# Kernel optimization log

Measured on AMD Instinct MI355X. Metric: run time of the kernel, lower is better.

Reference implementation:

```python
import jax, jax.numpy as jnp
import numpy as np

DIM = 1024
N_STATE = 64
T, B = 512, 32


def _xavier(key, shape):
    fan_out, fan_in = shape
    limit = np.sqrt(6.0 / (fan_in + fan_out)).astype(np.float32)
    return jax.random.uniform(key, shape, jnp.float32, -limit, limit)


def setup_inputs() -> dict:
    key = jax.random.key(0)
    ks = jax.random.split(key, 5)
    return {
        "x": jax.random.normal(ks[0], (T, B, DIM), jnp.float32),
        "S": jnp.zeros((B, N_STATE, N_STATE), jnp.float32),
        "W_k": _xavier(ks[1], (N_STATE, DIM)),
        "W_v": _xavier(ks[2], (N_STATE, DIM)),
        "W_q": _xavier(ks[3], (N_STATE, DIM)),
        "W_alpha": _xavier(ks[4], (N_STATE, DIM)),
        "d_alpha": jnp.full((N_STATE,), 0.1, jnp.float32),
        "b_alpha": jnp.full((N_STATE,), 2.0, jnp.float32),
    }


def reference(x, S, W_k, W_v, W_q, W_alpha, d_alpha, b_alpha):
    # Precompute all projections as batched GEMMs: [T,B,n_state]
    k = jnp.einsum("tbd,nd->tbn", x, W_k)
    v = jnp.einsum("tbd,nd->tbn", x, W_v)
    q = jnp.einsum("tbd,nd->tbn", x, W_q)
    ax = jnp.einsum("tbd,nd->tbn", x, W_alpha)

    def step(S, inp):
        k_t, v_t, q_t, ax_t = inp  # each [B, n_state]
        retrieved = jnp.einsum("bij,bj->bi", S, k_t)          # S @ k
        alpha = jax.nn.sigmoid(ax_t + d_alpha * retrieved + b_alpha)
        # S = alpha * S + (1 - alpha) * outer(v, k); alpha gates rows
        S_new = alpha[:, :, None] * S + (1.0 - alpha)[:, :, None] * (
            v_t[:, :, None] * k_t[:, None, :]
        )
        h = jnp.einsum("bij,bj->bi", S_new, q_t)              # S @ q
        out_t = h * jax.nn.silu(h)                             # self-gated output
        return S_new, out_t

    S_final, output = jax.lax.scan(step, S, (k, v, q, ax))
    return output, S_final
```

## Files before the change

kernel.cpp:

```cpp
#include <hip/hip_runtime.h>
#include <hip/hip_bf16.h>

#define T_STEPS 512
#define BATCH 32
#define NST 64
#define DIM 1024

typedef _Float16 f16x8 __attribute__((ext_vector_type(8)));
typedef _Float16 f16x4 __attribute__((ext_vector_type(4)));
typedef _Float16 f16x2 __attribute__((ext_vector_type(2)));
typedef float f32x4 __attribute__((ext_vector_type(4)));

__device__ __forceinline__ void gl_lds16(const void* g, void* l) {
  __builtin_amdgcn_global_load_lds(
      (const __attribute__((address_space(1))) void*)g,
      (__attribute__((address_space(3))) void*)l, 16, 0, 0);
}

__global__ __launch_bounds__(256) void wconv(
    const float* __restrict__ Wk, const float* __restrict__ Wv,
    const float* __restrict__ Wq, const float* __restrict__ Wa,
    _Float16* __restrict__ Wc) {
  const int n = blockIdx.x;
  const int g = n >> 6, r = n & 63;
  const float* W = (g == 0) ? Wk : (g == 1) ? Wq : (g == 2) ? Wv : Wa;
  float4 v = *(const float4*)(W + (size_t)r * DIM + threadIdx.x * 4);
  f16x4 h = {(_Float16)v.x, (_Float16)v.y, (_Float16)v.z, (_Float16)v.w};
  *(f16x4*)(Wc + (size_t)n * DIM + threadIdx.x * 4) = h;
}

__global__ __launch_bounds__(512) void proj_gemm(
    const float* __restrict__ x, const _Float16* __restrict__ Wc,
    _Float16* __restrict__ projh) {
  const int m0 = blockIdx.x * 64;
  const int tid = threadIdx.x;
  const int lane = tid & 63, wv = tid >> 6;
  const int wm = wv >> 2, wn = wv & 3;
  const int fm = lane & 15, fq = lane >> 4;

  __shared__ __align__(16) _Float16 Bl[2][256 * 32];
  __shared__ __align__(16) _Float16 Al[2][64 * 32];

  const int brow = tid >> 2;
  const int bcg = (tid & 3) ^ ((tid >> 3) & 3);
  const _Float16* gB = Wc + (size_t)brow * DIM + bcg * 8;
  const int bdst = tid * 8;

#define STAGE_B(buf, k0)                                          \
  {                                                               \
    _Pragma("unroll") for (int i = 0; i < 2; ++i)                 \
        gl_lds16(gB + (size_t)i * 128 * DIM + (k0),               \
                 &Bl[buf][i * 4096 + bdst]);                      \
  }

  const int arow = tid >> 3;
  const int afc = (tid & 7) * 4;
  const float* gA = x + (size_t)(m0 + arow) * DIM + afc;
  const int awp = arow * 32 + ((((tid >> 1) & 3) ^ ((arow >> 1) & 3)) * 8) +
                  (tid & 1) * 4;

#define LOADX(rr, k0)                          \
  {                                            \
    rr = *(const float4*)(gA + (k0));          \
  }
#define CVT_WRITE_A(buf, rr)                                        \
  {                                                                 \
    f16x4 h = {(_Float16)rr.x, (_Float16)rr.y, (_Float16)rr.z,      \
               (_Float16)rr.w};                                     \
    *(f16x4*)&Al[buf][awp] = h;                                     \
  }

  f32x4 acc[2][4];
#pragma unroll
  for (int mi = 0; mi < 2; ++mi)
#pragma unroll
    for (int ni = 0; ni < 4; ++ni) acc[mi][ni] = (f32x4){0.f, 0.f, 0.f, 0.f};

  const int aswz = (fq ^ ((fm >> 1) & 3)) * 8;
  const int abase = (wm * 32 + fm) * 32 + aswz;
  const int bbase = (wn * 64 + fm) * 32 + aswz;

#define COMPUTE(cb)                                                     \
  {                                                                     \
    f16x8 afr[2], bfr[4];                                               \
    _Pragma("unroll") for (int mi = 0; mi < 2; ++mi)                    \
        afr[mi] = *(const f16x8*)&Al[cb][abase + mi * 16 * 32];         \
    _Pragma("unroll") for (int ni = 0; ni < 4; ++ni)                    \
        bfr[ni] = *(const f16x8*)&Bl[cb][bbase + ni * 16 * 32];         \
    _Pragma("unroll") for (int mi = 0; mi < 2; ++mi)                    \
        _Pragma("unroll") for (int ni = 0; ni < 4; ++ni)                \
            acc[mi][ni] = __builtin_amdgcn_mfma_f32_16x16x32_f16(       \
                afr[mi], bfr[ni], acc[mi][ni], 0, 0, 0);                \
  }

  float4 rE, rO;
  LOADX(rE, 0);
  STAGE_B(0, 0);
  LOADX(rO, 32);
  CVT_WRITE_A(0, rE);
  __syncthreads();

  for (int k2 = 0; k2 < 16; ++k2) {
    STAGE_B(1, (2 * k2 + 1) * 32);
    if (k2 < 15) LOADX(rE, (2 * k2 + 2) * 32);
    CVT_WRITE_A(1, rO);
    COMPUTE(0);
    __syncthreads();
    if (k2 < 15) {
      STAGE_B(0, (2 * k2 + 2) * 32);
      LOADX(rO, (2 * k2 + 3) * 32);
      CVT_WRITE_A(0, rE);
    }
    COMPUTE(1);
    __syncthreads();
  }
#undef STAGE_B
#undef LOADX
#undef CVT_WRITE_A
#undef COMPUTE

#pragma unroll
  for (int mi = 0; mi < 2; ++mi)
#pragma unroll
    for (int ni = 0; ni < 4; ++ni) {
      const int gcol = wn * 64 + ni * 16 + fm;
      const int pcol = gcol < 128 ? gcol
                     : (gcol < 192 ? 128 + 2 * (gcol - 128) : 129 + 2 * (gcol - 192));
#pragma unroll
      for (int r = 0; r < 4; ++r) {
        const int grow = m0 + wm * 32 + mi * 16 + fq * 4 + r;
        projh[(size_t)grow * 256 + pcol] = (_Float16)acc[mi][ni][r];
      }
    }
}

__device__ __forceinline__ float red16(float x) {
  int v = __builtin_amdgcn_update_dpp(0, __float_as_int(x), 0xB1, 0xF, 0xF, true);
  x += __int_as_float(v);
  v = __builtin_amdgcn_update_dpp(0, __float_as_int(x), 0x4E, 0xF, 0xF, true);
  x += __int_as_float(v);
  v = __builtin_amdgcn_update_dpp(0, __float_as_int(x), 0x124, 0xF, 0xF, true);
  x += __int_as_float(v);
  v = __builtin_amdgcn_update_dpp(0, __float_as_int(x), 0x128, 0xF, 0xF, true);
  x += __int_as_float(v);
  return x;
}

__global__ __launch_bounds__(256) void scan_kernel(
    const _Float16* __restrict__ projh, const float* __restrict__ S0,
    const float* __restrict__ d_alpha, const float* __restrict__ b_alpha,
    float* __restrict__ out, float* __restrict__ Sout) {
  const int b = blockIdx.x >> 2;
  const int rg = blockIdx.x & 3;
  const int tid = threadIdx.x;
  const int c = tid & 15;
  const int r = rg * 16 + (tid >> 4);
  const int j0 = c * 4;

  __shared__ __align__(16) _Float16 lbuf[2 * 2048];

  float s[4];
  {
    float4 v = *(const float4*)(S0 + ((size_t)b * NST + r) * NST + j0);
    s[0] = v.x; s[1] = v.y; s[2] = v.z; s[3] = v.w;
  }
  const float da = d_alpha[r];
  const float ba = b_alpha[r];

  const _Float16* gp = projh + (size_t)b * 256;
  const int lidx = (tid >> 5) * 256 + (tid & 31) * 8;
#define GADDR(ch) (gp + (size_t)((ch) * 8 + (tid >> 5)) * (BATCH * 256) + (tid & 31) * 8)

  float4 rA;
  rA = *(const float4*)GADDR(0); *(float4*)(lbuf + lidx) = rA;
  rA = *(const float4*)GADDR(1); *(float4*)(lbuf + 2048 + lidx) = rA;
  rA = *(const float4*)GADDR(2);
  __syncthreads();

  f16x4 kf[2], qf[2];
  f16x2 vaf[2];
#define PREF(tn)                                                           \
  {                                                                        \
    const int pp = (tn)&1;                                                 \
    const _Float16* Pn = lbuf + (((tn) >> 3) & 1) * 2048 + ((tn)&7) * 256; \
    kf[pp] = *(const f16x4*)(Pn + j0);                                     \
    qf[pp] = *(const f16x4*)(Pn + 64 + j0);                                \
    vaf[pp] = *(const f16x2*)(Pn + 128 + 2 * r);                           \
  }

  PREF(0);
  for (int ch = 0; ch < 64; ++ch) {
#pragma unroll
    for (int si = 0; si < 8; ++si) {
      const int t = ch * 8 + si;
      const int p = t & 1;
      if (t + 1 < T_STEPS) PREF(t + 1);

      const float k0 = (float)kf[p][0], k1 = (float)kf[p][1];
      const float k2 = (float)kf[p][2], k3 = (float)kf[p][3];
      const float q0 = (float)qf[p][0], q1 = (float)qf[p][1];
      const float q2 = (float)qf[p][2], q3 = (float)qf[p][3];
      const float vi = (float)vaf[p][0];
      const float axv = (float)vaf[p][1];

      const float pa = fmaf(s[0], k0, s[1] * k1);
      const float pb = fmaf(s[2], k2, s[3] * k3);
      const float rr = red16(pa + pb);

      float z = fmaf(da, rr, axv + ba);
      z = fminf(fmaxf(z, -30.f), 30.f);
      const float e = __expf(-z);
      const float al = __builtin_amdgcn_rcpf(1.f + e);
      const float cc = (e * vi) * al;

      s[0] = fmaf(al, s[0], cc * k0);
      s[1] = fmaf(al, s[1], cc * k1);
      s[2] = fmaf(al, s[2], cc * k2);
      s[3] = fmaf(al, s[3], cc * k3);
      const float ha = fmaf(s[0], q0, s[1] * q1);
      const float hb = fmaf(s[2], q2, s[3] * q3);
      const float h = red16(ha + hb);

      if (c == 0) {
        const float sg = __builtin_amdgcn_rcpf(1.f + __expf(-h));
        out[((size_t)t * BATCH + b) * NST + r] = h * h * sg;
      }
    }
    if (ch + 2 < 64) {
      __syncthreads();
      *(float4*)(lbuf + (ch & 1) * 2048 + lidx) = rA;
      if (ch + 3 < 64) rA = *(const float4*)GADDR(ch + 3);
      __syncthreads();
    }
  }
#undef PREF
#undef GADDR

  float4 o = {s[0], s[1], s[2], s[3]};
  *(float4*)(Sout + ((size_t)b * NST + r) * NST + j0) = o;
}

extern "C" void kernel_launch(void* const* d_in, const int* in_sizes, int n_in,
                              void* d_out, int out_size, void* d_ws, size_t ws_size,
                              hipStream_t stream) {
  const float* x  = (const float*)d_in[0];
  const float* S0 = (const float*)d_in[1];
  const float* Wk = (const float*)d_in[2];
  const float* Wv = (const float*)d_in[3];
  const float* Wq = (const float*)d_in[4];
  const float* Wa = (const float*)d_in[5];
  const float* da = (const float*)d_in[6];
  const float* ba = (const float*)d_in[7];

  float* out  = (float*)d_out;
  float* Sout = out + (size_t)T_STEPS * BATCH * NST;
  _Float16* projh = (_Float16*)d_ws;
  _Float16* Wc = (_Float16*)((char*)d_ws + (size_t)16384 * 256 * 2);

  wconv<<<256, 256, 0, stream>>>(Wk, Wv, Wq, Wa, Wc);
  proj_gemm<<<256, 512, 0, stream>>>(x, Wc, projh);
  scan_kernel<<<4 * BATCH, 256, 0, stream>>>(projh, S0, da, ba, out, Sout);
}
```

Baseline: 224.9 us.

## Use fp32 projections, packed f32x2 math, exp2 sigmoid, and batched output epilogue

```diff
diff --git a/kernel.cpp b/kernel.cpp
--- a/kernel.cpp
+++ b/kernel.cpp
@@ -8,8 +8,8 @@
 
 typedef _Float16 f16x8 __attribute__((ext_vector_type(8)));
 typedef _Float16 f16x4 __attribute__((ext_vector_type(4)));
-typedef _Float16 f16x2 __attribute__((ext_vector_type(2)));
 typedef float f32x4 __attribute__((ext_vector_type(4)));
+typedef float f32x2 __attribute__((ext_vector_type(2)));
 
 __device__ __forceinline__ void gl_lds16(const void* g, void* l) {
   __builtin_amdgcn_global_load_lds(
@@ -24,14 +24,16 @@
   const int n = blockIdx.x;
   const int g = n >> 6, r = n & 63;
   const float* W = (g == 0) ? Wk : (g == 1) ? Wq : (g == 2) ? Wv : Wa;
+  const float sc = (g == 3) ? -1.44269504088896340736f : 1.0f;
   float4 v = *(const float4*)(W + (size_t)r * DIM + threadIdx.x * 4);
-  f16x4 h = {(_Float16)v.x, (_Float16)v.y, (_Float16)v.z, (_Float16)v.w};
+  f16x4 h = {(_Float16)(v.x * sc), (_Float16)(v.y * sc), (_Float16)(v.z * sc),
+             (_Float16)(v.w * sc)};
   *(f16x4*)(Wc + (size_t)n * DIM + threadIdx.x * 4) = h;
 }
 
 __global__ __launch_bounds__(512) void proj_gemm(
     const float* __restrict__ x, const _Float16* __restrict__ Wc,
-    _Float16* __restrict__ projh) {
+    float* __restrict__ projf) {
   const int m0 = blockIdx.x * 64;
   const int tid = threadIdx.x;
   const int lane = tid & 63, wv = tid >> 6;
@@ -129,7 +131,7 @@
 #pragma unroll
       for (int r = 0; r < 4; ++r) {
         const int grow = m0 + wm * 32 + mi * 16 + fq * 4 + r;
-        projh[(size_t)grow * 256 + pcol] = (_Float16)acc[mi][ni][r];
+        projf[(size_t)grow * 256 + pcol] = acc[mi][ni][r];
       }
     }
 }
@@ -146,46 +148,53 @@
   return x;
 }
 
-__global__ __launch_bounds__(256) void scan_kernel(
-    const _Float16* __restrict__ projh, const float* __restrict__ S0,
+__global__ __launch_bounds__(256, 1) void scan_kernel(
+    const float* __restrict__ projf, const float* __restrict__ S0,
     const float* __restrict__ d_alpha, const float* __restrict__ b_alpha,
     float* __restrict__ out, float* __restrict__ Sout) {
   const int b = blockIdx.x >> 2;
   const int rg = blockIdx.x & 3;
   const int tid = threadIdx.x;
   const int c = tid & 15;
-  const int r = rg * 16 + (tid >> 4);
+  const int lr = tid >> 4;
+  const int r = rg * 16 + lr;
   const int j0 = c * 4;
 
-  __shared__ __align__(16) _Float16 lbuf[2 * 2048];
-
-  float s[4];
+  __shared__ __align__(16) float lbuf[2 * 2048];
+  __shared__ __align__(16) float hbuf[8 * 16];
+
+  constexpr float NL2E = -1.44269504088896340736f;
+  f32x2 s01, s23;
   {
     float4 v = *(const float4*)(S0 + ((size_t)b * NST + r) * NST + j0);
-    s[0] = v.x; s[1] = v.y; s[2] = v.z; s[3] = v.w;
-  }
-  const float da = d_alpha[r];
-  const float ba = b_alpha[r];
-
-  const _Float16* gp = projh + (size_t)b * 256;
+    s01 = (f32x2){v.x, v.y}; s23 = (f32x2){v.z, v.w};
+  }
+  const float da2 = d_alpha[r] * NL2E;
+  const float ba2 = b_alpha[r] * NL2E;
+
+  const float* gp = projf + (size_t)b * 256;
   const int lidx = (tid >> 5) * 256 + (tid & 31) * 8;
 #define GADDR(ch) (gp + (size_t)((ch) * 8 + (tid >> 5)) * (BATCH * 256) + (tid & 31) * 8)
 
-  float4 rA;
-  rA = *(const float4*)GADDR(0); *(float4*)(lbuf + lidx) = rA;
-  rA = *(const float4*)GADDR(1); *(float4*)(lbuf + 2048 + lidx) = rA;
-  rA = *(const float4*)GADDR(2);
+  float4 rA0, rA1;
+  rA0 = *(const float4*)GADDR(0); rA1 = *(const float4*)(GADDR(0) + 4);
+  *(float4*)(lbuf + lidx) = rA0; *(float4*)(lbuf + lidx + 4) = rA1;
+  rA0 = *(const float4*)GADDR(1); rA1 = *(const float4*)(GADDR(1) + 4);
+  *(float4*)(lbuf + 2048 + lidx) = rA0; *(float4*)(lbuf + 2048 + lidx + 4) = rA1;
+  rA0 = *(const float4*)GADDR(2); rA1 = *(const float4*)(GADDR(2) + 4);
   __syncthreads();
 
-  f16x4 kf[2], qf[2];
-  f16x2 vaf[2];
-#define PREF(tn)                                                           \
-  {                                                                        \
-    const int pp = (tn)&1;                                                 \
-    const _Float16* Pn = lbuf + (((tn) >> 3) & 1) * 2048 + ((tn)&7) * 256; \
-    kf[pp] = *(const f16x4*)(Pn + j0);                                     \
-    qf[pp] = *(const f16x4*)(Pn + 64 + j0);                                \
-    vaf[pp] = *(const f16x2*)(Pn + 128 + 2 * r);                           \
+  f32x2 k01[2], k23[2], q01[2], q23[2], va[2];
+#define PREF(tn)                                                            \
+  {                                                                         \
+    const int pp = (tn) & 1;                                                \
+    const float* Pn = lbuf + (((tn) >> 3) & 1) * 2048 + ((tn) & 7) * 256;   \
+    float4 kk = *(const float4*)(Pn + j0);                                  \
+    float4 qq = *(const float4*)(Pn + 64 + j0);                             \
+    k01[pp] = (f32x2){kk.x, kk.y}; k23[pp] = (f32x2){kk.z, kk.w};           \
+    q01[pp] = (f32x2){qq.x, qq.y}; q23[pp] = (f32x2){qq.z, qq.w};           \
+    float2 vv = *(const float2*)(Pn + 128 + 2 * r);                         \
+    va[pp] = (f32x2){vv.x, vv.y};                                           \
   }
 
   PREF(0);
@@ -196,47 +205,49 @@
       const int p = t & 1;
       if (t + 1 < T_STEPS) PREF(t + 1);
 
-      const float k0 = (float)kf[p][0], k1 = (float)kf[p][1];
-      const float k2 = (float)kf[p][2], k3 = (float)kf[p][3];
-      const float q0 = (float)qf[p][0], q1 = (float)qf[p][1];
-      const float q2 = (float)qf[p][2], q3 = (float)qf[p][3];
-      const float vi = (float)vaf[p][0];
-      const float axv = (float)vaf[p][1];
-
-      const float pa = fmaf(s[0], k0, s[1] * k1);
-      const float pb = fmaf(s[2], k2, s[3] * k3);
-      const float rr = red16(pa + pb);
-
-      float z = fmaf(da, rr, axv + ba);
-      z = fminf(fmaxf(z, -30.f), 30.f);
-      const float e = __expf(-z);
+      f32x2 pa = s01 * k01[p] + s23 * k23[p];
+      const float rr = red16(pa[0] + pa[1]);
+
+      float z2 = fmaf(da2, rr, va[p][1] + ba2);
+      z2 = fminf(fmaxf(z2, -43.3f), 43.3f);
+      const float e = __builtin_amdgcn_exp2f(z2);
       const float al = __builtin_amdgcn_rcpf(1.f + e);
-      const float cc = (e * vi) * al;
-
-      s[0] = fmaf(al, s[0], cc * k0);
-      s[1] = fmaf(al, s[1], cc * k1);
-      s[2] = fmaf(al, s[2], cc * k2);
-      s[3] = fmaf(al, s[3], cc * k3);
-      const float ha = fmaf(s[0], q0, s[1] * q1);
-      const float hb = fmaf(s[2], q2, s[3] * q3);
-      const float h = red16(ha + hb);
-
-      if (c == 0) {
-        const float sg = __builtin_amdgcn_rcpf(1.f + __expf(-h));
-        out[((size_t)t * BATCH + b) * NST + r] = h * h * sg;
-      }
-    }
+      const float cc = (e * va[p][0]) * al;
+
+      const f32x2 al2 = {al, al}, cc2 = {cc, cc};
+      s01 = al2 * s01 + cc2 * k01[p];
+      s23 = al2 * s23 + cc2 * k23[p];
+
+      f32x2 hh = s01 * q01[p] + s23 * q23[p];
+      const float h = red16(hh[0] + hh[1]);
+      if (c == 0) hbuf[si * 16 + lr] = h;
+    }
+    __syncthreads();
     if (ch + 2 < 64) {
-      __syncthreads();
-      *(float4*)(lbuf + (ch & 1) * 2048 + lidx) = rA;
-      if (ch + 3 < 64) rA = *(const float4*)GADDR(ch + 3);
-      __syncthreads();
-    }
+      *(float4*)(lbuf + (ch & 1) * 2048 + lidx) = rA0;
+      *(float4*)(lbuf + (ch & 1) * 2048 + lidx + 4) = rA1;
+    }
+    if (tid < 64) {
+      const int tl = tid >> 3;
+      const int pr = (tid & 7) * 2;
+      float2 hv = *(const float2*)(hbuf + tl * 16 + pr);
+      const float e0 = __builtin_amdgcn_exp2f(hv.x * NL2E);
+      const float e1 = __builtin_amdgcn_exp2f(hv.y * NL2E);
+      float2 y;
+      y.x = (hv.x * hv.x) * __builtin_amdgcn_rcpf(1.f + e0);
+      y.y = (hv.y * hv.y) * __builtin_amdgcn_rcpf(1.f + e1);
+      *(float2*)(out + ((size_t)(ch * 8 + tl) * BATCH + b) * NST + rg * 16 + pr) = y;
+    }
+    if (ch + 3 < 64) {
+      rA0 = *(const float4*)GADDR(ch + 3);
+      rA1 = *(const float4*)(GADDR(ch + 3) + 4);
+    }
+    __syncthreads();
   }
 #undef PREF
 #undef GADDR
 
-  float4 o = {s[0], s[1], s[2], s[3]};
+  float4 o = {s01[0], s01[1], s23[0], s23[1]};
   *(float4*)(Sout + ((size_t)b * NST + r) * NST + j0) = o;
 }
 
@@ -254,10 +265,10 @@
 
   float* out  = (float*)d_out;
   float* Sout = out + (size_t)T_STEPS * BATCH * NST;
-  _Float16* projh = (_Float16*)d_ws;
-  _Float16* Wc = (_Float16*)((char*)d_ws + (size_t)16384 * 256 * 2);
+  float* projf = (float*)d_ws;
+  _Float16* Wc = (_Float16*)((char*)d_ws + (size_t)16384 * 256 * 4);
 
   wconv<<<256, 256, 0, stream>>>(Wk, Wv, Wq, Wa, Wc);
-  proj_gemm<<<256, 512, 0, stream>>>(x, Wc, projh);
-  scan_kernel<<<4 * BATCH, 256, 0, stream>>>(projh, S0, da, ba, out, Sout);
-}
+  proj_gemm<<<256, 512, 0, stream>>>(x, Wc, projf);
+  scan_kernel<<<4 * BATCH, 256, 0, stream>>>(projf, S0, da, ba, out, Sout);
+}
```

After: 218.2 us. 1.03x faster.
